# Kernel optimization log

Measured on AMD Instinct MI355X. Metric: run time of the kernel, lower is better.

The kernel has to match this reference:

```python
import jax, jax.numpy as jnp
import numpy as np

B, T, C = 2, 2048, 2048
N_HEAD, N_KV = 16, 4
HD = C // N_HEAD          # 128
ROPE_THETA = 10000.0


def setup_inputs() -> dict:
    key = jax.random.key(0)
    ks = jax.random.split(key, 6)
    std = 0.02
    x = jax.random.normal(ks[0], (B, T, C), dtype=jnp.float32)
    Wq = jax.random.normal(ks[1], (C, C), dtype=jnp.float32) * std
    Wk = jax.random.normal(ks[2], (C, N_KV * HD), dtype=jnp.float32) * std
    Wv = jax.random.normal(ks[3], (C, N_KV * HD), dtype=jnp.float32) * std
    Wo = jax.random.normal(ks[4], (C, C), dtype=jnp.float32) * std
    # real RoPE frequencies: freqs_cis = exp(i * t * theta^{-2j/hd})
    inv_freq = 1.0 / (ROPE_THETA ** (jnp.arange(0, HD, 2, dtype=jnp.float32) / HD))
    ang = jnp.arange(T, dtype=jnp.float32)[:, None] * inv_freq[None, :]  # [T, HD//2]
    return {"x": x, "Wq": Wq, "Wk": Wk, "Wv": Wv, "Wo": Wo,
            "freqs_cos": jnp.cos(ang), "freqs_sin": jnp.sin(ang)}


def _rope(t, cos, sin):
    # t: [B, H, T, HD]; cos/sin: [T, HD//2] -> complex rotate even/odd pairs
    tr = t.reshape(*t.shape[:-1], HD // 2, 2)
    re, im = tr[..., 0], tr[..., 1]
    c = cos[None, None, :, :]
    s = sin[None, None, :, :]
    out = jnp.stack([re * c - im * s, re * s + im * c], axis=-1)
    return out.reshape(t.shape)


def reference(x, Wq, Wk, Wv, Wo, freqs_cos, freqs_sin):
    Bm, Tm, Cm = x.shape
    q = (x @ Wq).reshape(Bm, Tm, N_HEAD, HD).transpose(0, 2, 1, 3)  # [B,H,T,HD]
    k = (x @ Wk).reshape(Bm, Tm, N_KV, HD).transpose(0, 2, 1, 3)    # [B,Hkv,T,HD]
    v = (x @ Wv).reshape(Bm, Tm, N_KV, HD).transpose(0, 2, 1, 3)
    q = _rope(q, freqs_cos, freqs_sin)
    k = _rope(k, freqs_cos, freqs_sin)
    rep = N_HEAD // N_KV
    k = jnp.repeat(k, rep, axis=1)  # GQA repeat_kv -> [B,H,T,HD]
    v = jnp.repeat(v, rep, axis=1)
    scale = 1.0 / jnp.sqrt(jnp.asarray(HD, dtype=x.dtype))
    att = jnp.einsum("bhqd,bhkd->bhqk", q, k) * scale
    causal = jnp.tril(jnp.ones((Tm, Tm), dtype=bool))
    att = jnp.where(causal[None, None], att, jnp.asarray(-jnp.inf, att.dtype))
    att = jax.nn.softmax(att, axis=-1)
    y = jnp.einsum("bhqk,bhkd->bhqd", att, v)
    y = y.transpose(0, 2, 1, 3).reshape(Bm, Tm, Cm)
    return y @ Wo
```

## Files before the change

kernel.cpp:

```cpp
#include <hip/hip_runtime.h>

#define B_ 2
#define T_ 2048
#define C_ 2048
#define NH_ 16
#define NKV_ 4
#define HD_ 128
#define REP_ (NH_ / NKV_)
#define LDQKV 3072

typedef unsigned short u16;
typedef __bf16 bf16x8v __attribute__((ext_vector_type(8)));
typedef float f32x4v __attribute__((ext_vector_type(4)));

__device__ __forceinline__ u16 f2bf(float f) {
    unsigned int u;
    __builtin_memcpy(&u, &f, 4);
    u += 0x7FFFu + ((u >> 16) & 1u);
    return (u16)(u >> 16);
}
__device__ __forceinline__ unsigned int pk2(float a, float b) {
    unsigned int ua, ub;
    __builtin_memcpy(&ua, &a, 4);
    __builtin_memcpy(&ub, &b, 4);
    ua += 0x8000u; ub += 0x8000u;
    return (ua >> 16) | (ub & 0xFFFF0000u);
}
__device__ __forceinline__ bf16x8v load8(const u16* p) {
    return *reinterpret_cast<const bf16x8v*>(p);
}
__device__ __forceinline__ void gl16(const u16* g, u16* l) {
    __builtin_amdgcn_global_load_lds(
        (const __attribute__((address_space(1))) void*)(g),
        (__attribute__((address_space(3))) void*)(l), 16, 0, 0);
}

__global__ void cvt_f32_bf16(const float* __restrict__ in, u16* __restrict__ out, int n4) {
    int i = blockIdx.x * blockDim.x + threadIdx.x;
    if (i >= n4) return;
    float4 v = reinterpret_cast<const float4*>(in)[i];
    ushort4 o;
    o.x = f2bf(v.x); o.y = f2bf(v.y); o.z = f2bf(v.z); o.w = f2bf(v.w);
    reinterpret_cast<ushort4*>(out)[i] = o;
}

__global__ void xpose_f32_bf16(const float* __restrict__ in, u16* __restrict__ out,
                               int R, int Cc) {
    __shared__ u16 tile[32][33];
    int bx = blockIdx.x * 32, by = blockIdx.y * 32;
    int tx = threadIdx.x, ty = threadIdx.y;
    for (int i = 0; i < 32; i += 8)
        tile[ty + i][tx] = f2bf(in[(size_t)(by + ty + i) * Cc + bx + tx]);
    __syncthreads();
    for (int i = 0; i < 32; i += 8)
        out[(size_t)(bx + ty + i) * R + by + tx] = tile[tx][ty + i];
}

__device__ __forceinline__ void stage_ab(const u16* gA, const u16* gB,
                                         u16* As, u16* Bs, int tid, int K) {
    u16* lA = As + tid * 8;
    u16* lB = Bs + tid * 8;
#pragma unroll
    for (int j = 0; j < 4; j++) gl16(gA + (size_t)(64 * j) * K, lA + j * 4096);
#pragma unroll
    for (int j = 0; j < 4; j++) gl16(gB + (size_t)(64 * j) * K, lB + j * 4096);
}

__global__ __launch_bounds__(512, 2) void gemm_qkv(const u16* __restrict__ A,
                                                   const u16* __restrict__ BT,
                                                   u16* __restrict__ Cq,
                                                   u16* __restrict__ vtb,
                                                   const float* __restrict__ cb,
                                                   const float* __restrict__ sb,
                                                   int M, int N, int K) {
    __shared__ __align__(16) u16 As[2][256 * 64];
    __shared__ __align__(16) u16 Bs[2][256 * 64];
    int tid = threadIdx.x;
    int lane = tid & 63, wave = tid >> 6;
    int wm = wave >> 2, wn = wave & 3;
    int m15 = lane & 15, quad = lane >> 4;

    int nbx = N >> 8;
    int nwg = gridDim.x;
    int bid = blockIdx.x;
    int cpx = nwg >> 3;
    int swz = (bid & 7) * cpx + (bid >> 3);
    int bx = swz % nbx, by = swz / nbx;
    int m0 = by * 256, n0 = bx * 256;

    int r_ = tid >> 3, c_ = tid & 7;
    const u16* gA = A + (size_t)(m0 + r_) * K + (c_ ^ (r_ & 7)) * 8;
    const u16* gB = BT + (size_t)(n0 + r_) * K + (c_ ^ (r_ & 7)) * 8;

    int sw8 = m15 & 7;
    const u16* a0b = &As[0][0] + (wm * 128 + m15) * 64;
    const u16* b0b = &Bs[0][0] + (wn * 64 + m15) * 64;

    f32x4v acc[8][4] = {};

    stage_ab(gA, gB, As[0], Bs[0], tid, K);
    __builtin_amdgcn_sched_barrier(0);
    stage_ab(gA + 64, gB + 64, As[1], Bs[1], tid, K);
    asm volatile("s_waitcnt vmcnt(8)" ::: "memory");
    __builtin_amdgcn_sched_barrier(0);
    __builtin_amdgcn_s_barrier();

    int NT = K >> 6;
    for (int t = 0; t < NT; t++) {
        const u16* a0 = a0b + (t & 1) * (256 * 64);
        const u16* b0 = b0b + (t & 1) * (256 * 64);
#pragma unroll
        for (int kc = 0; kc < 2; kc++) {
            int co = ((kc * 4 + quad) ^ sw8) * 8;
            bf16x8v bfv[4], af[8];
#pragma unroll
            for (int nt = 0; nt < 4; nt++) bfv[nt] = load8(b0 + nt * 1024 + co);
#pragma unroll
            for (int mt = 0; mt < 8; mt++) af[mt] = load8(a0 + mt * 1024 + co);
            __builtin_amdgcn_s_setprio(1);
#pragma unroll
            for (int mt = 0; mt < 8; mt++)
#pragma unroll
                for (int nt = 0; nt < 4; nt++)
                    acc[mt][nt] = __builtin_amdgcn_mfma_f32_16x16x32_bf16(
                        af[mt], bfv[nt], acc[mt][nt], 0, 0, 0);
            __builtin_amdgcn_s_setprio(0);
        }
        __builtin_amdgcn_s_barrier();
        if (t + 2 < NT) {
            stage_ab(gA + (t + 2) * 64, gB + (t + 2) * 64, As[t & 1], Bs[t & 1], tid, K);
            asm volatile("s_waitcnt vmcnt(8)" ::: "memory");
        } else {
            asm volatile("s_waitcnt vmcnt(0)" ::: "memory");
        }
        __builtin_amdgcn_sched_barrier(0);
        __builtin_amdgcn_s_barrier();
    }

    if (n0 >= 2560) {
#pragma unroll
        for (int mt = 0; mt < 8; mt++)
#pragma unroll
            for (int nt = 0; nt < 4; nt++) {
                int hd = n0 + wn * 64 + nt * 16 + m15 - 2560;
                int mbase = m0 + wm * 128 + mt * 16 + quad * 4;
                int bb = mbase >> 11, tok = mbase & 2047;
                int g = (tok & 31) >> 2;
                int off = (tok & ~31) + ((g & 3) * 8 + (g >> 2) * 4);
                ushort4 pk;
                pk.x = f2bf(acc[mt][nt][0]);
                pk.y = f2bf(acc[mt][nt][1]);
                pk.z = f2bf(acc[mt][nt][2]);
                pk.w = f2bf(acc[mt][nt][3]);
                *reinterpret_cast<ushort4*>(vtb + ((size_t)bb * 512 + hd) * T_ + off) = pk;
            }
    } else {
#pragma unroll
        for (int mt = 0; mt < 8; mt++)
#pragma unroll
            for (int nt = 0; nt < 4; nt++) {
                int c = n0 + wn * 64 + nt * 16 + m15;
                int i = (c & 127) >> 1;
                float sgn = (c & 1) ? 1.f : -1.f;
#pragma unroll
                for (int r = 0; r < 4; r++) {
                    int mrow = m0 + wm * 128 + mt * 16 + quad * 4 + r;
                    int tok = mrow & 2047;
                    float cv = cb[tok * 64 + i];
                    float sv = sb[tok * 64 + i];
                    float v = acc[mt][nt][r];
                    float pval = __shfl_xor(v, 1, 64);
                    float outv = fmaf(v, cv, pval * sv * sgn);
                    Cq[(size_t)mrow * N + c] = f2bf(outv);
                }
            }
    }
}

__global__ __launch_bounds__(512, 2) void gemm_out(const u16* __restrict__ A,
                                                   const u16* __restrict__ BT,
                                                   float* __restrict__ C,
                                                   int M, int N, int K) {
    __shared__ __align__(16) u16 As[2][256 * 64];
    __shared__ __align__(16) u16 Bs[2][256 * 64];
    int tid = threadIdx.x;
    int lane = tid & 63, wave = tid >> 6;
    int wm = wave >> 2, wn = wave & 3;
    int m15 = lane & 15, quad = lane >> 4;

    int nbx = N >> 8;
    int nwg = gridDim.x;
    int bid = blockIdx.x;
    int cpx = nwg >> 3;
    int swz = (bid & 7) * cpx + (bid >> 3);
    int bx = swz % nbx, by = swz / nbx;
    int m0 = by * 256, n0 = bx * 256;

    int r_ = tid >> 3, c_ = tid & 7;
    const u16* gA = A + (size_t)(m0 + r_) * K + (c_ ^ (r_ & 7)) * 8;
    const u16* gB = BT + (size_t)(n0 + r_) * K + (c_ ^ (r_ & 7)) * 8;

    int sw8 = m15 & 7;
    const u16* a0b = &As[0][0] + (wm * 128 + m15) * 64;
    const u16* b0b = &Bs[0][0] + (wn * 64 + m15) * 64;

    f32x4v acc[8][4] = {};

    stage_ab(gA, gB, As[0], Bs[0], tid, K);
    __builtin_amdgcn_sched_barrier(0);
    stage_ab(gA + 64, gB + 64, As[1], Bs[1], tid, K);
    asm volatile("s_waitcnt vmcnt(8)" ::: "memory");
    __builtin_amdgcn_sched_barrier(0);
    __builtin_amdgcn_s_barrier();

    int NT = K >> 6;
    for (int t = 0; t < NT; t++) {
        const u16* a0 = a0b + (t & 1) * (256 * 64);
        const u16* b0 = b0b + (t & 1) * (256 * 64);
#pragma unroll
        for (int kc = 0; kc < 2; kc++) {
            int co = ((kc * 4 + quad) ^ sw8) * 8;
            bf16x8v bfv[4], af[8];
#pragma unroll
            for (int nt = 0; nt < 4; nt++) bfv[nt] = load8(b0 + nt * 1024 + co);
#pragma unroll
            for (int mt = 0; mt < 8; mt++) af[mt] = load8(a0 + mt * 1024 + co);
            __builtin_amdgcn_s_setprio(1);
#pragma unroll
            for (int mt = 0; mt < 8; mt++)
#pragma unroll
                for (int nt = 0; nt < 4; nt++)
                    acc[mt][nt] = __builtin_amdgcn_mfma_f32_16x16x32_bf16(
                        af[mt], bfv[nt], acc[mt][nt], 0, 0, 0);
            __builtin_amdgcn_s_setprio(0);
        }
        __builtin_amdgcn_s_barrier();
        if (t + 2 < NT) {
            stage_ab(gA + (t + 2) * 64, gB + (t + 2) * 64, As[t & 1], Bs[t & 1], tid, K);
            asm volatile("s_waitcnt vmcnt(8)" ::: "memory");
        } else {
            asm volatile("s_waitcnt vmcnt(0)" ::: "memory");
        }
        __builtin_amdgcn_sched_barrier(0);
        __builtin_amdgcn_s_barrier();
    }

#pragma unroll
    for (int mt = 0; mt < 8; mt++)
#pragma unroll
        for (int nt = 0; nt < 4; nt++) {
            int c = n0 + wn * 64 + nt * 16 + m15;
#pragma unroll
            for (int r = 0; r < 4; r++) {
                int mrow = m0 + wm * 128 + mt * 16 + quad * 4 + r;
                C[(size_t)mrow * N + c] = acc[mt][nt][r];
            }
        }
}

__device__ __forceinline__ void stage_k128(const u16* kB, u16* Kl, int kt, int tid) {
    int keyc = tid >> 4, ch = tid & 15;
    const u16* g = kB + (size_t)(kt + keyc) * LDQKV + (ch ^ keyc) * 8;
    u16* l = Kl + tid * 8;
    for (int j = 0; j < 8; j++) {
        gl16(g, l);
        g += (size_t)16 * LDQKV;
        l += 2048;
    }
}
__device__ __forceinline__ void stage_v128(const u16* vB, u16* Vl, int kt, int tid) {
    int hdc = tid >> 4, ch = tid & 15;
    const u16* g = vB + (size_t)hdc * T_ + kt + (ch ^ hdc) * 8;
    u16* l = Vl + tid * 8;
    for (int j = 0; j < 8; j++) {
        gl16(g, l);
        g += (size_t)16 * T_;
        l += 2048;
    }
}

__global__ __launch_bounds__(256) void flash_k(const u16* __restrict__ qkv,
                                               const u16* __restrict__ vtb,
                                               u16* __restrict__ yb) {
    __shared__ __align__(16) u16 Kl[128 * 128];
    __shared__ __align__(16) u16 Vl[128 * 128];
    int h = blockIdx.y, b = blockIdx.z;
    int kv = h / REP_;
    int tid = threadIdx.x;
    int lane = tid & 63, wave = tid >> 6;
    int m15 = lane & 15, quad = lane >> 4;
    const u16* kB = qkv + (size_t)b * T_ * LDQKV + 2048 + kv * HD_;
    const u16* vB = vtb + ((size_t)(b * NKV_ + kv)) * HD_ * T_;
    const float scale2 = 0.1275173723f;
    const float M0b = 8.0f;
    const float NEG = -3.0e38f;

    for (int p = 0; p < 2; p++) {
        int qt = (p == 0) ? (int)blockIdx.x : (31 - (int)blockIdx.x);
        int qt0 = qt * 64;
        int qrow = qt0 + wave * 16;
        int q_i = qrow + m15;
        const u16* qp = qkv + (size_t)(b * T_ + q_i) * LDQKV + h * HD_ + quad * 8;
        bf16x8v qf[4];
        for (int kc = 0; kc < 4; kc++) qf[kc] = load8(qp + kc * 32);
        f32x4v o[8] = {};
        f32x4v lacc = {};

        int iters = qt0 / 128 + 1;
        for (int it = 0; it < iters; it++) {
            int kt = it * 128;
            __syncthreads();
            stage_k128(kB, Kl, kt, tid);
            stage_v128(vB, Vl, kt, tid);
            __syncthreads();
            f32x4v s4[8];
            for (int nt = 0; nt < 8; nt++) s4[nt] = (f32x4v){0.f, 0.f, 0.f, 0.f};
            for (int nt = 0; nt < 8; nt++) {
                const u16* kls = Kl + (nt * 16 + m15) * 128;
                for (int kc = 0; kc < 4; kc++)
                    s4[nt] = __builtin_amdgcn_mfma_f32_16x16x32_bf16(
                        load8(kls + (((kc * 4 + quad) ^ m15) * 8)), qf[kc], s4[nt], 0, 0, 0);
            }
            if (kt + 128 > qt0) {
                for (int nt = 0; nt < 8; nt++) {
                    int key = kt + nt * 16 + quad * 4;
                    for (int r = 0; r < 4; r++)
                        if (key + r > q_i) s4[nt][r] = NEG;
                }
            }
            for (int nt = 0; nt < 8; nt++) {
                for (int r = 0; r < 4; r++)
                    s4[nt][r] = exp2f(fmaf(s4[nt][r], scale2, -M0b));
                lacc += s4[nt];
            }
            for (int c = 0; c < 4; c++) {
                unsigned int w[4];
                w[0] = pk2(s4[2 * c][0], s4[2 * c][1]);
                w[1] = pk2(s4[2 * c][2], s4[2 * c][3]);
                w[2] = pk2(s4[2 * c + 1][0], s4[2 * c + 1][1]);
                w[3] = pk2(s4[2 * c + 1][2], s4[2 * c + 1][3]);
                bf16x8v pf;
                __builtin_memcpy(&pf, w, 16);
                for (int dt = 0; dt < 8; dt++) {
                    const u16* vls = Vl + (dt * 16 + m15) * 128;
                    o[dt] = __builtin_amdgcn_mfma_f32_16x16x32_bf16(
                        load8(vls + (((c * 4 + quad) ^ m15) * 8)), pf, o[dt], 0, 0, 0);
                }
            }
        }
        float l = lacc[0] + lacc[1] + lacc[2] + lacc[3];
        l += __shfl_xor(l, 16, 64);
        l += __shfl_xor(l, 32, 64);
        float inv = 1.f / l;
        u16* yp = yb + (size_t)(b * T_ + q_i) * C_ + h * HD_ + quad * 4;
        for (int dt = 0; dt < 8; dt++) {
            ushort4 pk;
            pk.x = f2bf(o[dt][0] * inv);
            pk.y = f2bf(o[dt][1] * inv);
            pk.z = f2bf(o[dt][2] * inv);
            pk.w = f2bf(o[dt][3] * inv);
            *reinterpret_cast<ushort4*>(yp + dt * 16) = pk;
        }
    }
}

extern "C" void kernel_launch(void* const* d_in, const int* in_sizes, int n_in,
                              void* d_out, int out_size, void* d_ws, size_t ws_size,
                              hipStream_t stream) {
    const float* x  = (const float*)d_in[0];
    const float* Wq = (const float*)d_in[1];
    const float* Wk = (const float*)d_in[2];
    const float* Wv = (const float*)d_in[3];
    const float* Wo = (const float*)d_in[4];
    const float* fc = (const float*)d_in[5];
    const float* fs = (const float*)d_in[6];
    float* out = (float*)d_out;

    char* ws = (char*)d_ws;
    u16* WqkvT = (u16*)(ws);
    u16* WoT   = (u16*)(ws + 12582912);
    u16* xb    = (u16*)(ws + 20971520);
    u16* qkvb  = (u16*)(ws + 37748736);
    u16* vtb   = (u16*)(ws + 62914560);
    u16* yb    = (u16*)(ws + 67108864);

    const int M = B_ * T_;

    int n4 = (M * C_) / 4;
    cvt_f32_bf16<<<n4 / 256, 256, 0, stream>>>(x, xb, n4);

    dim3 tb(32, 8);
    xpose_f32_bf16<<<dim3(C_ / 32, C_ / 32), tb, 0, stream>>>(Wq, WqkvT, C_, C_);
    xpose_f32_bf16<<<dim3((NKV_ * HD_) / 32, C_ / 32), tb, 0, stream>>>(Wk, WqkvT + 2048 * 2048, C_, NKV_ * HD_);
    xpose_f32_bf16<<<dim3((NKV_ * HD_) / 32, C_ / 32), tb, 0, stream>>>(Wv, WqkvT + 2560 * 2048, C_, NKV_ * HD_);
    xpose_f32_bf16<<<dim3(C_ / 32, C_ / 32), tb, 0, stream>>>(Wo, WoT, C_, C_);

    gemm_qkv<<<dim3((LDQKV / 256) * (M / 256)), 512, 0, stream>>>(xb, WqkvT, qkvb, vtb, fc, fs, M, LDQKV, C_);

    flash_k<<<dim3(T_ / 128, NH_, B_), 256, 0, stream>>>(qkvb, vtb, yb);

    gemm_out<<<dim3((C_ / 256) * (M / 256)), 512, 0, stream>>>(yb, WoT, out, M, C_, C_);
}
```

Baseline: 321.9 us.

## Split GEMM main loop into four MFMA quadrants interleaved with staged loads

Both projection GEMMs now run each K-step as four sub-phases (quadrants of the output tile). Each phase issues its own LDS fragment loads and global-to-LDS prefetch, separated by barriers and priority toggles, so memory traffic overlaps with MFMA work at a finer grain. The output GEMM also shrinks its M tile from 256 to 128, doubling the grid to improve occupancy and wave balance. The cost is many more barriers per iteration, and for the output GEMM lower data reuse per block.

```diff
diff --git a/kernel.cpp b/kernel.cpp
--- a/kernel.cpp
+++ b/kernel.cpp
@@ -34,6 +34,14 @@
         (const __attribute__((address_space(1))) void*)(g),
         (__attribute__((address_space(3))) void*)(l), 16, 0, 0);
 }
+__device__ __forceinline__ void stg(const u16* g, u16* l, int tid, int K) {
+    gl16(g, l + tid * 8);
+    gl16(g + (size_t)64 * K, l + 4096 + tid * 8);
+}
+#define BAR()      __builtin_amdgcn_s_barrier()
+#define LGKM0()    asm volatile("s_waitcnt lgkmcnt(0)" ::: "memory")
+#define SCHED0()   __builtin_amdgcn_sched_barrier(0)
+#define PRIO(x)    __builtin_amdgcn_s_setprio(x)
 
 __global__ void cvt_f32_bf16(const float* __restrict__ in, u16* __restrict__ out, int n4) {
     int i = blockIdx.x * blockDim.x + threadIdx.x;
@@ -56,16 +64,6 @@
         out[(size_t)(bx + ty + i) * R + by + tx] = tile[tx][ty + i];
 }
 
-__device__ __forceinline__ void stage_ab(const u16* gA, const u16* gB,
-                                         u16* As, u16* Bs, int tid, int K) {
-    u16* lA = As + tid * 8;
-    u16* lB = Bs + tid * 8;
-#pragma unroll
-    for (int j = 0; j < 4; j++) gl16(gA + (size_t)(64 * j) * K, lA + j * 4096);
-#pragma unroll
-    for (int j = 0; j < 4; j++) gl16(gB + (size_t)(64 * j) * K, lB + j * 4096);
-}
-
 __global__ __launch_bounds__(512, 2) void gemm_qkv(const u16* __restrict__ A,
                                                    const u16* __restrict__ BT,
                                                    u16* __restrict__ Cq,
@@ -73,68 +71,117 @@
                                                    const float* __restrict__ cb,
                                                    const float* __restrict__ sb,
                                                    int M, int N, int K) {
-    __shared__ __align__(16) u16 As[2][256 * 64];
-    __shared__ __align__(16) u16 Bs[2][256 * 64];
+    __shared__ __align__(16) u16 As[2][2][8192];
+    __shared__ __align__(16) u16 Bs[2][2][8192];
     int tid = threadIdx.x;
     int lane = tid & 63, wave = tid >> 6;
     int wm = wave >> 2, wn = wave & 3;
     int m15 = lane & 15, quad = lane >> 4;
 
     int nbx = N >> 8;
-    int nwg = gridDim.x;
-    int bid = blockIdx.x;
-    int cpx = nwg >> 3;
+    int bid = blockIdx.x, cpx = gridDim.x >> 3;
     int swz = (bid & 7) * cpx + (bid >> 3);
-    int bx = swz % nbx, by = swz / nbx;
-    int m0 = by * 256, n0 = bx * 256;
-
-    int r_ = tid >> 3, c_ = tid & 7;
-    const u16* gA = A + (size_t)(m0 + r_) * K + (c_ ^ (r_ & 7)) * 8;
-    const u16* gB = BT + (size_t)(n0 + r_) * K + (c_ ^ (r_ & 7)) * 8;
+    int m0 = (swz / nbx) * 256, n0 = (swz % nbx) * 256;
+
+    const u16* gA0 = A + (size_t)(m0 + (tid >> 3)) * K + (((tid & 7) ^ ((tid >> 3) & 7)) * 8);
+    const u16* gB0 = BT + (size_t)(n0 + (tid >> 3)) * K + (((tid & 7) ^ ((tid >> 3) & 7)) * 8);
 
     int sw8 = m15 & 7;
-    const u16* a0b = &As[0][0] + (wm * 128 + m15) * 64;
-    const u16* b0b = &Bs[0][0] + (wn * 64 + m15) * 64;
+    int co0 = (quad ^ sw8) * 8;
+    int co1 = ((4 + quad) ^ sw8) * 8;
+    const u16* aB = &As[0][0][0] + wm * 8192 + m15 * 64;
+    const u16* bB = &Bs[0][0][0] + (wn >> 1) * 8192 + ((wn & 1) * 64 + m15) * 64;
 
     f32x4v acc[8][4] = {};
-
-    stage_ab(gA, gB, As[0], Bs[0], tid, K);
-    __builtin_amdgcn_sched_barrier(0);
-    stage_ab(gA + 64, gB + 64, As[1], Bs[1], tid, K);
-    asm volatile("s_waitcnt vmcnt(8)" ::: "memory");
-    __builtin_amdgcn_sched_barrier(0);
-    __builtin_amdgcn_s_barrier();
-
     int NT = K >> 6;
+
+    stg(gB0, &Bs[0][0][0], tid, K);
+    stg(gB0 + (size_t)128 * K, &Bs[0][1][0], tid, K);
+    stg(gA0, &As[0][0][0], tid, K);
+    stg(gA0 + (size_t)128 * K, &As[0][1][0], tid, K);
+    stg(gB0 + 64, &Bs[1][0][0], tid, K);
+    stg(gB0 + (size_t)128 * K + 64, &Bs[1][1][0], tid, K);
+    asm volatile("s_waitcnt vmcnt(4)" ::: "memory");
+    SCHED0();
+    BAR();
+
     for (int t = 0; t < NT; t++) {
-        const u16* a0 = a0b + (t & 1) * (256 * 64);
-        const u16* b0 = b0b + (t & 1) * (256 * 64);
-#pragma unroll
-        for (int kc = 0; kc < 2; kc++) {
-            int co = ((kc * 4 + quad) ^ sw8) * 8;
-            bf16x8v bfv[4], af[8];
-#pragma unroll
-            for (int nt = 0; nt < 4; nt++) bfv[nt] = load8(b0 + nt * 1024 + co);
-#pragma unroll
-            for (int mt = 0; mt < 8; mt++) af[mt] = load8(a0 + mt * 1024 + co);
-            __builtin_amdgcn_s_setprio(1);
-#pragma unroll
-            for (int mt = 0; mt < 8; mt++)
-#pragma unroll
-                for (int nt = 0; nt < 4; nt++)
+        int d = t & 1;
+        const u16* aT = aB + d * 16384;
+        const u16* bT = bB + d * 16384;
+        bf16x8v a0[4][2], a1[4][2], b0[2][2], b1[2][2];
+
+#pragma unroll
+        for (int mt = 0; mt < 4; mt++) {
+            a0[mt][0] = load8(aT + mt * 1024 + co0);
+            a0[mt][1] = load8(aT + mt * 1024 + co1);
+        }
+#pragma unroll
+        for (int nt = 0; nt < 2; nt++) {
+            b0[nt][0] = load8(bT + nt * 1024 + co0);
+            b0[nt][1] = load8(bT + nt * 1024 + co1);
+        }
+        if (t + 1 < NT) stg(gA0 + (t + 1) * 64, &As[1 - d][0][0], tid, K);
+        BAR(); LGKM0(); SCHED0(); PRIO(1);
+#pragma unroll
+        for (int kc = 0; kc < 2; kc++)
+#pragma unroll
+            for (int mt = 0; mt < 4; mt++)
+#pragma unroll
+                for (int nt = 0; nt < 2; nt++)
                     acc[mt][nt] = __builtin_amdgcn_mfma_f32_16x16x32_bf16(
-                        af[mt], bfv[nt], acc[mt][nt], 0, 0, 0);
-            __builtin_amdgcn_s_setprio(0);
-        }
-        __builtin_amdgcn_s_barrier();
-        if (t + 2 < NT) {
-            stage_ab(gA + (t + 2) * 64, gB + (t + 2) * 64, As[t & 1], Bs[t & 1], tid, K);
-            asm volatile("s_waitcnt vmcnt(8)" ::: "memory");
-        } else {
-            asm volatile("s_waitcnt vmcnt(0)" ::: "memory");
-        }
-        __builtin_amdgcn_sched_barrier(0);
-        __builtin_amdgcn_s_barrier();
+                        a0[mt][kc], b0[nt][kc], acc[mt][nt], 0, 0, 0);
+        PRIO(0); BAR();
+
+#pragma unroll
+        for (int nt = 0; nt < 2; nt++) {
+            b1[nt][0] = load8(bT + (nt + 2) * 1024 + co0);
+            b1[nt][1] = load8(bT + (nt + 2) * 1024 + co1);
+        }
+        if (t + 1 < NT) stg(gA0 + (size_t)128 * K + (t + 1) * 64, &As[1 - d][1][0], tid, K);
+        BAR(); LGKM0(); SCHED0(); PRIO(1);
+#pragma unroll
+        for (int kc = 0; kc < 2; kc++)
+#pragma unroll
+            for (int mt = 0; mt < 4; mt++)
+#pragma unroll
+                for (int nt = 0; nt < 2; nt++)
+                    acc[mt][nt + 2] = __builtin_amdgcn_mfma_f32_16x16x32_bf16(
+                        a0[mt][kc], b1[nt][kc], acc[mt][nt + 2], 0, 0, 0);
+        PRIO(0); BAR();
+
+#pragma unroll
+        for (int mt = 0; mt < 4; mt++) {
+            a1[mt][0] = load8(aT + (mt + 4) * 1024 + co0);
+            a1[mt][1] = load8(aT + (mt + 4) * 1024 + co1);
+        }
+        if (t + 2 < NT) stg(gB0 + (t + 2) * 64, &Bs[d][0][0], tid, K);
+        BAR(); LGKM0(); SCHED0(); PRIO(1);
+#pragma unroll
+        for (int kc = 0; kc < 2; kc++)
+#pragma unroll
+            for (int mt = 0; mt < 4; mt++)
+#pragma unroll
+                for (int nt = 0; nt < 2; nt++)
+                    acc[mt + 4][nt] = __builtin_amdgcn_mfma_f32_16x16x32_bf16(
+                        a1[mt][kc], b0[nt][kc], acc[mt + 4][nt], 0, 0, 0);
+        PRIO(0); BAR();
+
+        if (t + 2 < NT) stg(gB0 + (size_t)128 * K + (t + 2) * 64, &Bs[d][1][0], tid, K);
+        BAR(); PRIO(1);
+#pragma unroll
+        for (int kc = 0; kc < 2; kc++)
+#pragma unroll
+            for (int mt = 0; mt < 4; mt++)
+#pragma unroll
+                for (int nt = 0; nt < 2; nt++)
+                    acc[mt + 4][nt + 2] = __builtin_amdgcn_mfma_f32_16x16x32_bf16(
+                        a1[mt][kc], b1[nt][kc], acc[mt + 4][nt + 2], 0, 0, 0);
+        PRIO(0);
+        if (t + 2 < NT) { asm volatile("s_waitcnt vmcnt(4)" ::: "memory"); }
+        else            { asm volatile("s_waitcnt vmcnt(0)" ::: "memory"); }
+        SCHED0();
+        BAR();
     }
 
     if (n0 >= 2560) {
@@ -181,78 +228,125 @@
                                                    const u16* __restrict__ BT,
                                                    float* __restrict__ C,
                                                    int M, int N, int K) {
-    __shared__ __align__(16) u16 As[2][256 * 64];
-    __shared__ __align__(16) u16 Bs[2][256 * 64];
+    __shared__ __align__(16) u16 As2[2][8192];
+    __shared__ __align__(16) u16 Bs2[2][2][8192];
     int tid = threadIdx.x;
     int lane = tid & 63, wave = tid >> 6;
     int wm = wave >> 2, wn = wave & 3;
     int m15 = lane & 15, quad = lane >> 4;
 
     int nbx = N >> 8;
-    int nwg = gridDim.x;
-    int bid = blockIdx.x;
-    int cpx = nwg >> 3;
+    int bid = blockIdx.x, cpx = gridDim.x >> 3;
     int swz = (bid & 7) * cpx + (bid >> 3);
-    int bx = swz % nbx, by = swz / nbx;
-    int m0 = by * 256, n0 = bx * 256;
-
-    int r_ = tid >> 3, c_ = tid & 7;
-    const u16* gA = A + (size_t)(m0 + r_) * K + (c_ ^ (r_ & 7)) * 8;
-    const u16* gB = BT + (size_t)(n0 + r_) * K + (c_ ^ (r_ & 7)) * 8;
+    int m0 = (swz / nbx) * 128, n0 = (swz % nbx) * 256;
+
+    const u16* gA0 = A + (size_t)(m0 + (tid >> 3)) * K + (((tid & 7) ^ ((tid >> 3) & 7)) * 8);
+    const u16* gB0 = BT + (size_t)(n0 + (tid >> 3)) * K + (((tid & 7) ^ ((tid >> 3) & 7)) * 8);
 
     int sw8 = m15 & 7;
-    const u16* a0b = &As[0][0] + (wm * 128 + m15) * 64;
-    const u16* b0b = &Bs[0][0] + (wn * 64 + m15) * 64;
-
-    f32x4v acc[8][4] = {};
-
-    stage_ab(gA, gB, As[0], Bs[0], tid, K);
-    __builtin_amdgcn_sched_barrier(0);
-    stage_ab(gA + 64, gB + 64, As[1], Bs[1], tid, K);
-    asm volatile("s_waitcnt vmcnt(8)" ::: "memory");
-    __builtin_amdgcn_sched_barrier(0);
-    __builtin_amdgcn_s_barrier();
-
+    int co0 = (quad ^ sw8) * 8;
+    int co1 = ((4 + quad) ^ sw8) * 8;
+    const u16* aB = &As2[0][0] + (wm * 64 + m15) * 64;
+    const u16* bB = &Bs2[0][0][0] + (wn >> 1) * 8192 + ((wn & 1) * 64 + m15) * 64;
+
+    f32x4v acc[4][4] = {};
     int NT = K >> 6;
+
+    stg(gB0, &Bs2[0][0][0], tid, K);
+    stg(gB0 + (size_t)128 * K, &Bs2[0][1][0], tid, K);
+    stg(gA0, &As2[0][0], tid, K);
+    stg(gB0 + 64, &Bs2[1][0][0], tid, K);
+    stg(gB0 + (size_t)128 * K + 64, &Bs2[1][1][0], tid, K);
+    asm volatile("s_waitcnt vmcnt(4)" ::: "memory");
+    SCHED0();
+    BAR();
+
     for (int t = 0; t < NT; t++) {
-        const u16* a0 = a0b + (t & 1) * (256 * 64);
-        const u16* b0 = b0b + (t & 1) * (256 * 64);
-#pragma unroll
-        for (int kc = 0; kc < 2; kc++) {
-            int co = ((kc * 4 + quad) ^ sw8) * 8;
-            bf16x8v bfv[4], af[8];
-#pragma unroll
-            for (int nt = 0; nt < 4; nt++) bfv[nt] = load8(b0 + nt * 1024 + co);
-#pragma unroll
-            for (int mt = 0; mt < 8; mt++) af[mt] = load8(a0 + mt * 1024 + co);
-            __builtin_amdgcn_s_setprio(1);
-#pragma unroll
-            for (int mt = 0; mt < 8; mt++)
-#pragma unroll
-                for (int nt = 0; nt < 4; nt++)
+        int d = t & 1;
+        const u16* aT = aB + d * 8192;
+        const u16* bT = bB + d * 16384;
+        bf16x8v a0[2][2], a1[2][2], b0[2][2], b1[2][2];
+
+#pragma unroll
+        for (int mt = 0; mt < 2; mt++) {
+            a0[mt][0] = load8(aT + mt * 1024 + co0);
+            a0[mt][1] = load8(aT + mt * 1024 + co1);
+        }
+#pragma unroll
+        for (int nt = 0; nt < 2; nt++) {
+            b0[nt][0] = load8(bT + nt * 1024 + co0);
+            b0[nt][1] = load8(bT + nt * 1024 + co1);
+        }
+        if (t + 1 < NT) stg(gA0 + (t + 1) * 64, &As2[1 - d][0], tid, K);
+        BAR(); LGKM0(); SCHED0(); PRIO(1);
+#pragma unroll
+        for (int kc = 0; kc < 2; kc++)
+#pragma unroll
+            for (int mt = 0; mt < 2; mt++)
+#pragma unroll
+                for (int nt = 0; nt < 2; nt++)
                     acc[mt][nt] = __builtin_amdgcn_mfma_f32_16x16x32_bf16(
-                        af[mt], bfv[nt], acc[mt][nt], 0, 0, 0);
-            __builtin_amdgcn_s_setprio(0);
-        }
-        __builtin_amdgcn_s_barrier();
-        if (t + 2 < NT) {
-            stage_ab(gA + (t + 2) * 64, gB + (t + 2) * 64, As[t & 1], Bs[t & 1], tid, K);
-            asm volatile("s_waitcnt vmcnt(8)" ::: "memory");
-        } else {
-            asm volatile("s_waitcnt vmcnt(0)" ::: "memory");
-        }
-        __builtin_amdgcn_sched_barrier(0);
-        __builtin_amdgcn_s_barrier();
-    }
-
-#pragma unroll
-    for (int mt = 0; mt < 8; mt++)
+                        a0[mt][kc], b0[nt][kc], acc[mt][nt], 0, 0, 0);
+        PRIO(0); BAR();
+
+#pragma unroll
+        for (int nt = 0; nt < 2; nt++) {
+            b1[nt][0] = load8(bT + (nt + 2) * 1024 + co0);
+            b1[nt][1] = load8(bT + (nt + 2) * 1024 + co1);
+        }
+        BAR(); LGKM0(); SCHED0(); PRIO(1);
+#pragma unroll
+        for (int kc = 0; kc < 2; kc++)
+#pragma unroll
+            for (int mt = 0; mt < 2; mt++)
+#pragma unroll
+                for (int nt = 0; nt < 2; nt++)
+                    acc[mt][nt + 2] = __builtin_amdgcn_mfma_f32_16x16x32_bf16(
+                        a0[mt][kc], b1[nt][kc], acc[mt][nt + 2], 0, 0, 0);
+        PRIO(0); BAR();
+
+#pragma unroll
+        for (int mt = 0; mt < 2; mt++) {
+            a1[mt][0] = load8(aT + (mt + 2) * 1024 + co0);
+            a1[mt][1] = load8(aT + (mt + 2) * 1024 + co1);
+        }
+        if (t + 2 < NT) stg(gB0 + (t + 2) * 64, &Bs2[d][0][0], tid, K);
+        BAR(); LGKM0(); SCHED0(); PRIO(1);
+#pragma unroll
+        for (int kc = 0; kc < 2; kc++)
+#pragma unroll
+            for (int mt = 0; mt < 2; mt++)
+#pragma unroll
+                for (int nt = 0; nt < 2; nt++)
+                    acc[mt + 2][nt] = __builtin_amdgcn_mfma_f32_16x16x32_bf16(
+                        a1[mt][kc], b0[nt][kc], acc[mt + 2][nt], 0, 0, 0);
+        PRIO(0); BAR();
+
+        if (t + 2 < NT) stg(gB0 + (size_t)128 * K + (t + 2) * 64, &Bs2[d][1][0], tid, K);
+        BAR(); PRIO(1);
+#pragma unroll
+        for (int kc = 0; kc < 2; kc++)
+#pragma unroll
+            for (int mt = 0; mt < 2; mt++)
+#pragma unroll
+                for (int nt = 0; nt < 2; nt++)
+                    acc[mt + 2][nt + 2] = __builtin_amdgcn_mfma_f32_16x16x32_bf16(
+                        a1[mt][kc], b1[nt][kc], acc[mt + 2][nt + 2], 0, 0, 0);
+        PRIO(0);
+        if (t + 2 < NT) { asm volatile("s_waitcnt vmcnt(4)" ::: "memory"); }
+        else            { asm volatile("s_waitcnt vmcnt(0)" ::: "memory"); }
+        SCHED0();
+        BAR();
+    }
+
+#pragma unroll
+    for (int mt = 0; mt < 4; mt++)
 #pragma unroll
         for (int nt = 0; nt < 4; nt++) {
             int c = n0 + wn * 64 + nt * 16 + m15;
 #pragma unroll
             for (int r = 0; r < 4; r++) {
-                int mrow = m0 + wm * 128 + mt * 16 + quad * 4 + r;
+                int mrow = m0 + wm * 64 + mt * 16 + quad * 4 + r;
                 C[(size_t)mrow * N + c] = acc[mt][nt][r];
             }
         }
@@ -399,5 +493,5 @@
 
     flash_k<<<dim3(T_ / 128, NH_, B_), 256, 0, stream>>>(qkvb, vtb, yb);
 
-    gemm_out<<<dim3((C_ / 256) * (M / 256)), 512, 0, stream>>>(yb, WoT, out, M, C_, C_);
-}
+    gemm_out<<<dim3((C_ / 256) * (M / 128)), 512, 0, stream>>>(yb, WoT, out, M, C_, C_);
+}
```

Result: faster. 297.6 us (-7.5%).
